# Performance work log

Measured on AMD Instinct MI355X. Metric: run time of the kernel, lower is better.

## Reference

```python
import jax, jax.numpy as jnp
import numpy as np

N_NODES = 100000
N_EDGES = 1600000
D_IN = 64
D_OUT = 64


def setup_inputs() -> dict:
    key = jax.random.key(0)
    k1, k2, k3, k4, k5 = jax.random.split(key, 5)
    features = jax.random.normal(k1, (N_NODES, D_IN), dtype=jnp.float32)
    edge_row = jax.random.randint(k2, (N_EDGES,), 0, N_NODES, dtype=jnp.int32)
    edge_col = jax.random.randint(k3, (N_EDGES,), 0, N_NODES, dtype=jnp.int32)
    edge_val = jax.random.uniform(k4, (N_EDGES,), dtype=jnp.float32)
    # learned parameters (xavier-uniform kernel, zero bias, ones skip weight)
    limit = float(np.sqrt(6.0 / (D_IN + D_OUT)))
    kernel = jax.random.uniform(k5, (D_IN, D_OUT), minval=-limit, maxval=limit, dtype=jnp.float32)
    bias = jnp.zeros((D_OUT,), dtype=jnp.float32)
    skip_weight = jnp.ones((D_OUT,), dtype=jnp.float32)
    return {
        "features": features,
        "kernel": kernel,
        "bias": bias,
        "skip_weight": skip_weight,
        "edge_row": edge_row,
        "edge_col": edge_col,
        "edge_val": edge_val,
    }


def reference(features, kernel, bias, skip_weight, edge_row, edge_col, edge_val):
    # dense projection: [n, d_in] @ [d_in, d_out]
    h = features @ kernel
    # SpMM: (A h)[r] = sum_{edges e with row r} val_e * h[col_e]
    gathered = h[edge_col] * edge_val[:, None]  # [n_edges, d_out]
    agg = jax.ops.segment_sum(gathered, edge_row, num_segments=N_NODES)
    out = h * skip_weight + agg + bias
    return jax.nn.selu(out)
```

## Files before the change

kernel.cpp:

```cpp
#include <hip/hip_runtime.h>
#include <math.h>

#define N_NODES 100000
#define N_EDGES 1600000
#define D 64
#define RPB 128
#define NBUK 782
#define CAP 3072
#define NGB 782
#define NHB 784
#define EPB 2048
#define POFF_ROW 784

typedef unsigned int u32;
typedef unsigned short u16;

static __device__ __forceinline__ u32 f2bf(float x) {
    u32 u = __float_as_uint(x);
    u32 r = u + 0x7FFFu + ((u >> 16) & 1u);
    return r >> 16;
}
static __device__ __forceinline__ u32 pack2(float a, float b) {
    return f2bf(a) | (f2bf(b) << 16);
}
static __device__ __forceinline__ float bflo(u32 u) { return __uint_as_float(u << 16); }
static __device__ __forceinline__ float bfhi(u32 u) { return __uint_as_float(u & 0xFFFF0000u); }
static __device__ __forceinline__ float selu(float x) {
    const float scale = 1.0507009873554805f;
    const float alpha = 1.6732632423543772f;
    return x > 0.f ? scale * x : scale * alpha * (expf(x) - 1.f);
}
static __device__ __forceinline__ u32 wave_iscan(u32 x, int lane) {
    #pragma unroll
    for (int d = 1; d < 64; d <<= 1) {
        u32 y = __shfl_up(x, d, 64);
        if (lane >= d) x += y;
    }
    return x;
}

__global__ __launch_bounds__(256) void fused_gemm_sort(
    const float* __restrict__ feat, const float* __restrict__ kern,
    const int* __restrict__ erow, const int* __restrict__ ecol,
    const float* __restrict__ eval, u16* __restrict__ hbf,
    int2* __restrict__ sedge, u32* __restrict__ poff)
{
    __shared__ u32 smem[4400];
    const int t = threadIdx.x;

    if (blockIdx.x >= NHB) {
        float* ks = (float*)smem;
        {
            const float4* k4 = (const float4*)kern;
            float4* ks4 = (float4*)ks;
            #pragma unroll
            for (int i = 0; i < 4; i++) ks4[t + 256 * i] = k4[t + 256 * i];
        }
        __syncthreads();

        const int cgi  = t & 7;
        const int rg   = t >> 3;
        const int row0 = (blockIdx.x - NHB) * RPB + rg * 4;

        float4 acc[4][2];
        #pragma unroll
        for (int r = 0; r < 4; r++)
            #pragma unroll
            for (int i = 0; i < 2; i++)
                acc[r][i] = make_float4(0.f, 0.f, 0.f, 0.f);

        #pragma unroll 4
        for (int s = 0; s < 16; s++) {
            float4 f[4];
            #pragma unroll
            for (int r = 0; r < 4; r++) {
                int row = min(row0 + r, N_NODES - 1);
                f[r] = ((const float4*)(feat + (size_t)row * D))[s];
            }
            float4 kk[4][2];
            #pragma unroll
            for (int kv = 0; kv < 4; kv++)
                #pragma unroll
                for (int i = 0; i < 2; i++)
                    kk[kv][i] = ((const float4*)(ks + (s * 4 + kv) * D))[cgi * 2 + i];
            #pragma unroll
            for (int r = 0; r < 4; r++) {
                #pragma unroll
                for (int kv = 0; kv < 4; kv++) {
                    float fv = (&f[r].x)[kv];
                    #pragma unroll
                    for (int i = 0; i < 2; i++) {
                        acc[r][i].x += fv * kk[kv][i].x;
                        acc[r][i].y += fv * kk[kv][i].y;
                        acc[r][i].z += fv * kk[kv][i].z;
                        acc[r][i].w += fv * kk[kv][i].w;
                    }
                }
            }
        }

        #pragma unroll
        for (int r = 0; r < 4; r++) {
            int row = row0 + r;
            if (row < N_NODES) {
                uint4 o;
                o.x = pack2(acc[r][0].x, acc[r][0].y);
                o.y = pack2(acc[r][0].z, acc[r][0].w);
                o.z = pack2(acc[r][1].x, acc[r][1].y);
                o.w = pack2(acc[r][1].z, acc[r][1].w);
                ((uint4*)(hbf + (size_t)row * D))[cgi] = o;
            }
        }
    } else {
        u32* er   = smem;
        u32* c    = er + EPB;
        u32* o    = c + NBUK;
        u32* cu   = o + NBUK + 1;
        u32* part = cu + NBUK;

        for (int i = t; i < NBUK; i += 256) c[i] = 0u;
        __syncthreads();

        const int hb   = blockIdx.x;
        const int base = hb * EPB;
        const int lane = t & 63;
        const int w    = t >> 6;

        #pragma unroll
        for (int k = 0; k < 8; k++) {
            int i = base + k * 256 + t;
            u32 r = 0xFFFFFFFFu;
            if (i < N_EDGES) { r = (u32)erow[i]; atomicAdd(&c[r >> 7], 1u); }
            er[k * 256 + t] = r;
        }
        __syncthreads();

        const int i0 = t * 4;
        u32 p = 0u;
        #pragma unroll
        for (int jj = 0; jj < 4; jj++) { int i = i0 + jj; if (i < NBUK) p += c[i]; }
        u32 incl = wave_iscan(p, lane);
        if (lane == 63) part[w] = incl;
        __syncthreads();
        {
            u32 wp = 0u;
            #pragma unroll
            for (int ww = 0; ww < 4; ww++) if (ww < w) wp += part[ww];
            u32 run = incl - p + wp;
            #pragma unroll
            for (int jj = 0; jj < 4; jj++) {
                int i = i0 + jj;
                if (i < NBUK) { o[i] = run; cu[i] = run; run += c[i]; }
            }
            if (t == 0) o[NBUK] = part[0] + part[1] + part[2] + part[3];
        }
        __syncthreads();

        #pragma unroll
        for (int k = 0; k < 8; k++) {
            int i = base + k * 256 + t;
            u32 r = er[k * 256 + t];
            if (r != 0xFFFFFFFFu) {
                u32 rk = atomicAdd(&cu[r >> 7], 1u);
                sedge[(size_t)hb * EPB + rk] =
                    make_int2(ecol[i] | (int)((r & 127u) << 17),
                              __float_as_int(eval[i]));
            }
        }

        for (int i = t; i <= NBUK; i += 256)
            poff[(size_t)hb * POFF_ROW + i] = o[i];
    }
}

__global__ __launch_bounds__(1024) void agg_kernel(
    const u32* __restrict__ poff, const int2* __restrict__ sedge,
    const u16* __restrict__ hbf, const float* __restrict__ skip,
    const float* __restrict__ bias, float* __restrict__ out)
{
    __shared__ int2 eA[CAP];
    __shared__ int2 eB[CAP];
    __shared__ u32 c[RPB];
    __shared__ u32 o[RPB];
    __shared__ u32 cur[RPB];
    __shared__ u32 combo[NHB];
    __shared__ u16 runid[CAP];
    __shared__ u32 wsum[16];
    __shared__ u32 wpre[16];
    __shared__ u32 cnt_sh;

    const int t = threadIdx.x;
    const int lane = t & 63;
    const int w = t >> 6;
    const int b = blockIdx.x;

    if (t < RPB) c[t] = 0u;

    u32 mylen = 0u, s0 = 0u;
    if (t < NHB) {
        const u32* pr = poff + (size_t)t * POFF_ROW + b;
        s0    = pr[0];
        mylen = pr[1] - s0;
    }
    u32 incl = wave_iscan(mylen, lane);
    if (lane == 63) wsum[w] = incl;
    __syncthreads();
    if (w == 0) {
        u32 v = (lane < 16) ? wsum[lane] : 0u;
        u32 pp = wave_iscan(v, lane);
        if (lane < 16) wpre[lane] = pp - v;
        if (lane == 15) cnt_sh = min(pp, (u32)CAP);
    }
    __syncthreads();
    incl += wpre[w];
    const u32 excl = incl - mylen;
    if (t < NHB) {
        combo[t] = s0 - excl;
        for (u32 j = excl; j < incl; j++)
            if (j < (u32)CAP) runid[j] = (u16)t;
    }
    __syncthreads();

    const u32 cnt = cnt_sh;

    for (u32 j = (u32)t; j < cnt; j += 1024u) {
        u32 rid = (u32)runid[j];
        u32 src = rid * (u32)EPB + combo[rid] + j;
        int2 e = sedge[(size_t)src];
        eA[j] = e;
        atomicAdd(&c[(u32)e.x >> 17], 1u);
    }
    __syncthreads();

    {
        u32 x = (t < RPB) ? c[t] : 0u;
        u32 ri = wave_iscan(x, lane);
        if (lane == 63) wsum[w] = ri;
        __syncthreads();
        if (t < RPB) {
            u32 add = (w == 1) ? wsum[0] : 0u;
            u32 e = ri + add - x;
            o[t] = e; cur[t] = e;
        }
        __syncthreads();
    }

    for (u32 j = (u32)t; j < cnt; j += 1024u) {
        int2 e = eA[j];
        u32 rl = (u32)e.x >> 17;
        u32 rk = atomicAdd(&cur[rl], 1u);
        eB[rk] = make_int2(e.x & 0x1FFFF, e.y);
    }
    __syncthreads();

    const int rows = min(RPB, N_NODES - b * RPB);
    const int g  = t >> 3;
    const int dg = t & 7;

    float a0 = 0.f, a1 = 0.f, a2 = 0.f, a3 = 0.f;
    float a4 = 0.f, a5 = 0.f, a6 = 0.f, a7 = 0.f;

    u32 jb = 0u, jend = 0u;
    if (g < rows) {
        jb = o[g];
        jend = min(jb + c[g], (u32)CAP);
    }

    u32 j = jb;
    for (; j + 3u < jend; j += 4u) {
        int2 e0 = eB[j];
        int2 e1 = eB[j + 1u];
        int2 e2 = eB[j + 2u];
        int2 e3 = eB[j + 3u];
        float v0 = __int_as_float(e0.y);
        float v1 = __int_as_float(e1.y);
        float v2 = __int_as_float(e2.y);
        float v3 = __int_as_float(e3.y);
        uint4 h0 = ((const uint4*)(hbf + (size_t)e0.x * D))[dg];
        uint4 h1 = ((const uint4*)(hbf + (size_t)e1.x * D))[dg];
        uint4 h2 = ((const uint4*)(hbf + (size_t)e2.x * D))[dg];
        uint4 h3 = ((const uint4*)(hbf + (size_t)e3.x * D))[dg];
        a0 += v0 * bflo(h0.x); a1 += v0 * bfhi(h0.x);
        a2 += v0 * bflo(h0.y); a3 += v0 * bfhi(h0.y);
        a4 += v0 * bflo(h0.z); a5 += v0 * bfhi(h0.z);
        a6 += v0 * bflo(h0.w); a7 += v0 * bfhi(h0.w);
        a0 += v1 * bflo(h1.x); a1 += v1 * bfhi(h1.x);
        a2 += v1 * bflo(h1.y); a3 += v1 * bfhi(h1.y);
        a4 += v1 * bflo(h1.z); a5 += v1 * bfhi(h1.z);
        a6 += v1 * bflo(h1.w); a7 += v1 * bfhi(h1.w);
        a0 += v2 * bflo(h2.x); a1 += v2 * bfhi(h2.x);
        a2 += v2 * bflo(h2.y); a3 += v2 * bfhi(h2.y);
        a4 += v2 * bflo(h2.z); a5 += v2 * bfhi(h2.z);
        a6 += v2 * bflo(h2.w); a7 += v2 * bfhi(h2.w);
        a0 += v3 * bflo(h3.x); a1 += v3 * bfhi(h3.x);
        a2 += v3 * bflo(h3.y); a3 += v3 * bfhi(h3.y);
        a4 += v3 * bflo(h3.z); a5 += v3 * bfhi(h3.z);
        a6 += v3 * bflo(h3.w); a7 += v3 * bfhi(h3.w);
    }
    for (; j < jend; j++) {
        int2 e0 = eB[j];
        float v0 = __int_as_float(e0.y);
        uint4 h0 = ((const uint4*)(hbf + (size_t)e0.x * D))[dg];
        a0 += v0 * bflo(h0.x); a1 += v0 * bfhi(h0.x);
        a2 += v0 * bflo(h0.y); a3 += v0 * bfhi(h0.y);
        a4 += v0 * bflo(h0.z); a5 += v0 * bfhi(h0.z);
        a6 += v0 * bflo(h0.w); a7 += v0 * bfhi(h0.w);
    }

    if (g < rows) {
        const int grow = b * RPB + g;
        uint4 hr = ((const uint4*)(hbf + (size_t)grow * D))[dg];
        float4 s0v = ((const float4*)skip)[2 * dg];
        float4 s1v = ((const float4*)skip)[2 * dg + 1];
        float4 b0v = ((const float4*)bias)[2 * dg];
        float4 b1v = ((const float4*)bias)[2 * dg + 1];
        float4 x0, x1;
        x0.x = selu(bflo(hr.x) * s0v.x + b0v.x + a0);
        x0.y = selu(bfhi(hr.x) * s0v.y + b0v.y + a1);
        x0.z = selu(bflo(hr.y) * s0v.z + b0v.z + a2);
        x0.w = selu(bfhi(hr.y) * s0v.w + b0v.w + a3);
        x1.x = selu(bflo(hr.z) * s1v.x + b1v.x + a4);
        x1.y = selu(bfhi(hr.z) * s1v.y + b1v.y + a5);
        x1.z = selu(bflo(hr.w) * s1v.z + b1v.z + a6);
        x1.w = selu(bfhi(hr.w) * s1v.w + b1v.w + a7);
        ((float4*)(out + (size_t)grow * D))[2 * dg]     = x0;
        ((float4*)(out + (size_t)grow * D))[2 * dg + 1] = x1;
    }
}

extern "C" void kernel_launch(void* const* d_in, const int* in_sizes, int n_in,
                              void* d_out, int out_size, void* d_ws, size_t ws_size,
                              hipStream_t stream)
{
    const float* feat = (const float*)d_in[0];
    const float* kern = (const float*)d_in[1];
    const float* bias = (const float*)d_in[2];
    const float* skip = (const float*)d_in[3];
    const int*   erow = (const int*)d_in[4];
    const int*   ecol = (const int*)d_in[5];
    const float* eval = (const float*)d_in[6];
    float* out = (float*)d_out;

    u16*  hbf   = (u16*)d_ws;
    u32*  poff  = (u32*)(hbf + (size_t)N_NODES * D);
    int2* sedge = (int2*)(poff + (size_t)NHB * POFF_ROW);

    hipLaunchKernelGGL(fused_gemm_sort, dim3(NGB + NHB), dim3(256), 0, stream,
                       feat, kern, erow, ecol, eval, hbf, sedge, poff);
    hipLaunchKernelGGL(agg_kernel, dim3(NBUK), dim3(1024), 0, stream,
                       poff, sedge, hbf, skip, bias, out);
}
```

Baseline: 166.2 us.

## Stage sorted edges in LDS, degree-sort rows, software-pipeline gather loop

The sort kernel no longer keeps row ids in shared memory. It re-reads erow in the scatter pass and scatters edges into an LDS tile, then writes the tile out coalesced instead of doing random global writes. The aggregation kernel counting-sorts the block's rows by degree so each wave handles rows of similar length, which reduces divergence. It also double-buffers the gather loads across iterations and sets a min-blocks launch bound. The trade-offs are a second global read of erow, extra LDS, and higher register pressure, which the launch bound may force into spills.

```diff
diff --git a/kernel.cpp b/kernel.cpp
--- a/kernel.cpp
+++ b/kernel.cpp
@@ -45,7 +45,7 @@
     const float* __restrict__ eval, u16* __restrict__ hbf,
     int2* __restrict__ sedge, u32* __restrict__ poff)
 {
-    __shared__ u32 smem[4400];
+    __shared__ u32 smem[5665];
     const int t = threadIdx.x;
 
     if (blockIdx.x >= NHB) {
@@ -112,13 +112,12 @@
             }
         }
     } else {
-        u32* er   = smem;
-        u32* c    = er + EPB;
-        u32* o    = c + NBUK;
-        u32* cu   = o + NBUK + 1;
-        u32* part = cu + NBUK;
-
-        for (int i = t; i < NBUK; i += 256) c[i] = 0u;
+        int2* tile = (int2*)smem;
+        u32* co    = smem + 4096;
+        u32* cu    = co + 783;
+        u32* part  = cu + 782;
+
+        for (int i = t; i < 783; i += 256) co[i] = 0u;
         __syncthreads();
 
         const int hb   = blockIdx.x;
@@ -129,16 +128,14 @@
         #pragma unroll
         for (int k = 0; k < 8; k++) {
             int i = base + k * 256 + t;
-            u32 r = 0xFFFFFFFFu;
-            if (i < N_EDGES) { r = (u32)erow[i]; atomicAdd(&c[r >> 7], 1u); }
-            er[k * 256 + t] = r;
+            if (i < N_EDGES) atomicAdd(&co[(u32)erow[i] >> 7], 1u);
         }
         __syncthreads();
 
         const int i0 = t * 4;
         u32 p = 0u;
         #pragma unroll
-        for (int jj = 0; jj < 4; jj++) { int i = i0 + jj; if (i < NBUK) p += c[i]; }
+        for (int jj = 0; jj < 4; jj++) { int i = i0 + jj; if (i < NBUK) p += co[i]; }
         u32 incl = wave_iscan(p, lane);
         if (lane == 63) part[w] = incl;
         __syncthreads();
@@ -150,30 +147,34 @@
             #pragma unroll
             for (int jj = 0; jj < 4; jj++) {
                 int i = i0 + jj;
-                if (i < NBUK) { o[i] = run; cu[i] = run; run += c[i]; }
-            }
-            if (t == 0) o[NBUK] = part[0] + part[1] + part[2] + part[3];
+                if (i < NBUK) { u32 cv = co[i]; co[i] = run; cu[i] = run; run += cv; }
+            }
+            if (t == 0) co[NBUK] = part[0] + part[1] + part[2] + part[3];
         }
         __syncthreads();
 
         #pragma unroll
         for (int k = 0; k < 8; k++) {
             int i = base + k * 256 + t;
-            u32 r = er[k * 256 + t];
-            if (r != 0xFFFFFFFFu) {
+            if (i < N_EDGES) {
+                u32 r = (u32)erow[i];
                 u32 rk = atomicAdd(&cu[r >> 7], 1u);
-                sedge[(size_t)hb * EPB + rk] =
-                    make_int2(ecol[i] | (int)((r & 127u) << 17),
-                              __float_as_int(eval[i]));
-            }
-        }
+                tile[rk] = make_int2(ecol[i] | (int)((r & 127u) << 17),
+                                     __float_as_int(eval[i]));
+            }
+        }
+        __syncthreads();
+
+        #pragma unroll
+        for (int k = 0; k < 8; k++)
+            sedge[(size_t)hb * EPB + k * 256 + t] = tile[k * 256 + t];
 
         for (int i = t; i <= NBUK; i += 256)
-            poff[(size_t)hb * POFF_ROW + i] = o[i];
-    }
-}
-
-__global__ __launch_bounds__(1024) void agg_kernel(
+            poff[(size_t)hb * POFF_ROW + i] = co[i];
+    }
+}
+
+__global__ __launch_bounds__(1024, 8) void agg_kernel(
     const u32* __restrict__ poff, const int2* __restrict__ sedge,
     const u16* __restrict__ hbf, const float* __restrict__ skip,
     const float* __restrict__ bias, float* __restrict__ out)
@@ -187,6 +188,8 @@
     __shared__ u16 runid[CAP];
     __shared__ u32 wsum[16];
     __shared__ u32 wpre[16];
+    __shared__ u32 dbin[64];
+    __shared__ u32 perm[RPB];
     __shared__ u32 cnt_sh;
 
     const int t = threadIdx.x;
@@ -195,6 +198,7 @@
     const int b = blockIdx.x;
 
     if (t < RPB) c[t] = 0u;
+    if (t < 64) dbin[t] = 0u;
 
     u32 mylen = 0u, s0 = 0u;
     if (t < NHB) {
@@ -245,6 +249,8 @@
         __syncthreads();
     }
 
+    if (t < RPB) atomicAdd(&dbin[min(c[t], 63u)], 1u);
+
     for (u32 j = (u32)t; j < cnt; j += 1024u) {
         int2 e = eA[j];
         u32 rl = (u32)e.x >> 17;
@@ -253,6 +259,18 @@
     }
     __syncthreads();
 
+    if (w == 0) {
+        u32 v = dbin[lane];
+        u32 sc = wave_iscan(v, lane);
+        dbin[lane] = sc - v;
+    }
+    __syncthreads();
+    if (t < RPB) {
+        u32 r = atomicAdd(&dbin[min(c[t], 63u)], 1u);
+        perm[r] = (u32)t;
+    }
+    __syncthreads();
+
     const int rows = min(RPB, N_NODES - b * RPB);
     const int g  = t >> 3;
     const int dg = t & 7;
@@ -260,55 +278,57 @@
     float a0 = 0.f, a1 = 0.f, a2 = 0.f, a3 = 0.f;
     float a4 = 0.f, a5 = 0.f, a6 = 0.f, a7 = 0.f;
 
-    u32 jb = 0u, jend = 0u;
-    if (g < rows) {
-        jb = o[g];
-        jend = min(jb + c[g], (u32)CAP);
-    }
+    const u32 rl = perm[g];
+    u32 jb   = o[rl];
+    u32 jend = min(jb + c[rl], (u32)CAP);
+
+#define LD4(J, H0,H1,H2,H3, V0,V1,V2,V3) do {                         \
+        int2 _e0 = eB[(J)];   int2 _e1 = eB[(J)+1u];                  \
+        int2 _e2 = eB[(J)+2u]; int2 _e3 = eB[(J)+3u];                 \
+        V0 = __int_as_float(_e0.y); V1 = __int_as_float(_e1.y);       \
+        V2 = __int_as_float(_e2.y); V3 = __int_as_float(_e3.y);       \
+        H0 = ((const uint4*)(hbf + (size_t)_e0.x * D))[dg];           \
+        H1 = ((const uint4*)(hbf + (size_t)_e1.x * D))[dg];           \
+        H2 = ((const uint4*)(hbf + (size_t)_e2.x * D))[dg];           \
+        H3 = ((const uint4*)(hbf + (size_t)_e3.x * D))[dg];           \
+    } while (0)
+#define FMA1(H, V) do {                                               \
+        a0 += (V) * bflo((H).x); a1 += (V) * bfhi((H).x);             \
+        a2 += (V) * bflo((H).y); a3 += (V) * bfhi((H).y);             \
+        a4 += (V) * bflo((H).z); a5 += (V) * bfhi((H).z);             \
+        a6 += (V) * bflo((H).w); a7 += (V) * bfhi((H).w);             \
+    } while (0)
 
     u32 j = jb;
-    for (; j + 3u < jend; j += 4u) {
-        int2 e0 = eB[j];
-        int2 e1 = eB[j + 1u];
-        int2 e2 = eB[j + 2u];
-        int2 e3 = eB[j + 3u];
-        float v0 = __int_as_float(e0.y);
-        float v1 = __int_as_float(e1.y);
-        float v2 = __int_as_float(e2.y);
-        float v3 = __int_as_float(e3.y);
-        uint4 h0 = ((const uint4*)(hbf + (size_t)e0.x * D))[dg];
-        uint4 h1 = ((const uint4*)(hbf + (size_t)e1.x * D))[dg];
-        uint4 h2 = ((const uint4*)(hbf + (size_t)e2.x * D))[dg];
-        uint4 h3 = ((const uint4*)(hbf + (size_t)e3.x * D))[dg];
-        a0 += v0 * bflo(h0.x); a1 += v0 * bfhi(h0.x);
-        a2 += v0 * bflo(h0.y); a3 += v0 * bfhi(h0.y);
-        a4 += v0 * bflo(h0.z); a5 += v0 * bfhi(h0.z);
-        a6 += v0 * bflo(h0.w); a7 += v0 * bfhi(h0.w);
-        a0 += v1 * bflo(h1.x); a1 += v1 * bfhi(h1.x);
-        a2 += v1 * bflo(h1.y); a3 += v1 * bfhi(h1.y);
-        a4 += v1 * bflo(h1.z); a5 += v1 * bfhi(h1.z);
-        a6 += v1 * bflo(h1.w); a7 += v1 * bfhi(h1.w);
-        a0 += v2 * bflo(h2.x); a1 += v2 * bfhi(h2.x);
-        a2 += v2 * bflo(h2.y); a3 += v2 * bfhi(h2.y);
-        a4 += v2 * bflo(h2.z); a5 += v2 * bfhi(h2.z);
-        a6 += v2 * bflo(h2.w); a7 += v2 * bfhi(h2.w);
-        a0 += v3 * bflo(h3.x); a1 += v3 * bfhi(h3.x);
-        a2 += v3 * bflo(h3.y); a3 += v3 * bfhi(h3.y);
-        a4 += v3 * bflo(h3.z); a5 += v3 * bfhi(h3.z);
-        a6 += v3 * bflo(h3.w); a7 += v3 * bfhi(h3.w);
+    {
+        uint4 hA0, hA1, hA2, hA3, hB0, hB1, hB2, hB3;
+        float vA0, vA1, vA2, vA3, vB0, vB1, vB2, vB3;
+        if (j + 3u < jend) {
+            LD4(j, hA0, hA1, hA2, hA3, vA0, vA1, vA2, vA3);
+            j += 4u;
+            while (j + 3u < jend) {
+                LD4(j, hB0, hB1, hB2, hB3, vB0, vB1, vB2, vB3);
+                FMA1(hA0, vA0); FMA1(hA1, vA1);
+                FMA1(hA2, vA2); FMA1(hA3, vA3);
+                hA0 = hB0; hA1 = hB1; hA2 = hB2; hA3 = hB3;
+                vA0 = vB0; vA1 = vB1; vA2 = vB2; vA3 = vB3;
+                j += 4u;
+            }
+            FMA1(hA0, vA0); FMA1(hA1, vA1);
+            FMA1(hA2, vA2); FMA1(hA3, vA3);
+        }
     }
     for (; j < jend; j++) {
         int2 e0 = eB[j];
         float v0 = __int_as_float(e0.y);
         uint4 h0 = ((const uint4*)(hbf + (size_t)e0.x * D))[dg];
-        a0 += v0 * bflo(h0.x); a1 += v0 * bfhi(h0.x);
-        a2 += v0 * bflo(h0.y); a3 += v0 * bfhi(h0.y);
-        a4 += v0 * bflo(h0.z); a5 += v0 * bfhi(h0.z);
-        a6 += v0 * bflo(h0.w); a7 += v0 * bfhi(h0.w);
-    }
-
-    if (g < rows) {
-        const int grow = b * RPB + g;
+        FMA1(h0, v0);
+    }
+#undef LD4
+#undef FMA1
+
+    if (rl < (u32)rows) {
+        const int grow = b * RPB + (int)rl;
         uint4 hr = ((const uint4*)(hbf + (size_t)grow * D))[dg];
         float4 s0v = ((const float4*)skip)[2 * dg];
         float4 s1v = ((const float4*)skip)[2 * dg + 1];
```

New measurement: 161.9 us. 2.6% less time.

## Stage bucket-sorted edges in LDS for coalesced stores; drop eA buffer

Applied to the files above, without the earlier changes.

The sort blocks now scatter edges into an LDS tile and write the finished 2048-edge tile to global memory with coalesced stores, instead of scattering directly to global. Row indices are re-read from global rather than cached in LDS, and the offsets share the count array in place. In the aggregation kernel the eA shared staging buffer is removed and sedge is re-read from global (likely L2-resident) on the second pass, freeing 24KB of LDS per block. The trade is extra global reads for fewer scattered writes and lower LDS use, which may allow higher occupancy.

```diff
diff --git a/kernel.cpp b/kernel.cpp
--- a/kernel.cpp
+++ b/kernel.cpp
@@ -45,7 +45,7 @@
     const float* __restrict__ eval, u16* __restrict__ hbf,
     int2* __restrict__ sedge, u32* __restrict__ poff)
 {
-    __shared__ u32 smem[4400];
+    __shared__ u32 smem[5665];
     const int t = threadIdx.x;
 
     if (blockIdx.x >= NHB) {
@@ -112,13 +112,12 @@
             }
         }
     } else {
-        u32* er   = smem;
-        u32* c    = er + EPB;
-        u32* o    = c + NBUK;
-        u32* cu   = o + NBUK + 1;
-        u32* part = cu + NBUK;
-
-        for (int i = t; i < NBUK; i += 256) c[i] = 0u;
+        int2* tile = (int2*)smem;
+        u32* co    = smem + 4096;
+        u32* cu    = co + 783;
+        u32* part  = cu + 782;
+
+        for (int i = t; i < 783; i += 256) co[i] = 0u;
         __syncthreads();
 
         const int hb   = blockIdx.x;
@@ -129,16 +128,14 @@
         #pragma unroll
         for (int k = 0; k < 8; k++) {
             int i = base + k * 256 + t;
-            u32 r = 0xFFFFFFFFu;
-            if (i < N_EDGES) { r = (u32)erow[i]; atomicAdd(&c[r >> 7], 1u); }
-            er[k * 256 + t] = r;
+            if (i < N_EDGES) atomicAdd(&co[(u32)erow[i] >> 7], 1u);
         }
         __syncthreads();
 
         const int i0 = t * 4;
         u32 p = 0u;
         #pragma unroll
-        for (int jj = 0; jj < 4; jj++) { int i = i0 + jj; if (i < NBUK) p += c[i]; }
+        for (int jj = 0; jj < 4; jj++) { int i = i0 + jj; if (i < NBUK) p += co[i]; }
         u32 incl = wave_iscan(p, lane);
         if (lane == 63) part[w] = incl;
         __syncthreads();
@@ -150,26 +147,30 @@
             #pragma unroll
             for (int jj = 0; jj < 4; jj++) {
                 int i = i0 + jj;
-                if (i < NBUK) { o[i] = run; cu[i] = run; run += c[i]; }
-            }
-            if (t == 0) o[NBUK] = part[0] + part[1] + part[2] + part[3];
+                if (i < NBUK) { u32 cv = co[i]; co[i] = run; cu[i] = run; run += cv; }
+            }
+            if (t == 0) co[NBUK] = part[0] + part[1] + part[2] + part[3];
         }
         __syncthreads();
 
         #pragma unroll
         for (int k = 0; k < 8; k++) {
             int i = base + k * 256 + t;
-            u32 r = er[k * 256 + t];
-            if (r != 0xFFFFFFFFu) {
+            if (i < N_EDGES) {
+                u32 r = (u32)erow[i];
                 u32 rk = atomicAdd(&cu[r >> 7], 1u);
-                sedge[(size_t)hb * EPB + rk] =
-                    make_int2(ecol[i] | (int)((r & 127u) << 17),
-                              __float_as_int(eval[i]));
-            }
-        }
+                tile[rk] = make_int2(ecol[i] | (int)((r & 127u) << 17),
+                                     __float_as_int(eval[i]));
+            }
+        }
+        __syncthreads();
+
+        #pragma unroll
+        for (int k = 0; k < 8; k++)
+            sedge[(size_t)hb * EPB + k * 256 + t] = tile[k * 256 + t];
 
         for (int i = t; i <= NBUK; i += 256)
-            poff[(size_t)hb * POFF_ROW + i] = o[i];
+            poff[(size_t)hb * POFF_ROW + i] = co[i];
     }
 }
 
@@ -178,7 +179,6 @@
     const u16* __restrict__ hbf, const float* __restrict__ skip,
     const float* __restrict__ bias, float* __restrict__ out)
 {
-    __shared__ int2 eA[CAP];
     __shared__ int2 eB[CAP];
     __shared__ u32 c[RPB];
     __shared__ u32 o[RPB];
@@ -227,7 +227,6 @@
         u32 rid = (u32)runid[j];
         u32 src = rid * (u32)EPB + combo[rid] + j;
         int2 e = sedge[(size_t)src];
-        eA[j] = e;
         atomicAdd(&c[(u32)e.x >> 17], 1u);
     }
     __syncthreads();
@@ -246,7 +245,9 @@
     }
 
     for (u32 j = (u32)t; j < cnt; j += 1024u) {
-        int2 e = eA[j];
+        u32 rid = (u32)runid[j];
+        u32 src = rid * (u32)EPB + combo[rid] + j;
+        int2 e = sedge[(size_t)src];
         u32 rl = (u32)e.x >> 17;
         u32 rk = atomicAdd(&cur[rl], 1u);
         eB[rk] = make_int2(e.x & 0x1FFFF, e.y);
```

Measured after the change: 170.2 us. +2.4%, slower.
